# Kernel optimization log

Measured on AMD Instinct MI355X. Metric: run time of the kernel, lower is better.

## Reference

```python
import jax, jax.numpy as jnp
import numpy as np
import math

B, S, D = 2, 2048, 1024
H, DH = 16, 64          # n_heads, d_head = d_model // n_heads
WINDOW = 256            # window_size


def setup_inputs() -> dict:
    key = jax.random.key(0)
    ks = jax.random.split(key, 9)
    scale = 0.02
    return {
        "x":  jax.random.normal(ks[0], (B, S, D), dtype=jnp.float32),
        "wq": jax.random.normal(ks[1], (D, D), dtype=jnp.float32) * scale,
        "bq": jnp.zeros((D,), dtype=jnp.float32),
        "wk": jax.random.normal(ks[2], (D, D), dtype=jnp.float32) * scale,
        "bk": jnp.zeros((D,), dtype=jnp.float32),
        "wv": jax.random.normal(ks[3], (D, D), dtype=jnp.float32) * scale,
        "bv": jnp.zeros((D,), dtype=jnp.float32),
        "wo": jax.random.normal(ks[4], (D, D), dtype=jnp.float32) * scale,
        "bo": jnp.zeros((D,), dtype=jnp.float32),
    }


def reference(x, wq, bq, wk, bk, wv, bv, wo, bo):
    b, s, d = x.shape
    # QKV projections -> [b, h, s, dh]
    q = (x @ wq + bq).reshape(b, s, H, DH).transpose(0, 2, 1, 3)
    k = (x @ wk + bk).reshape(b, s, H, DH).transpose(0, 2, 1, 3)
    v = (x @ wv + bv).reshape(b, s, H, DH).transpose(0, 2, 1, 3)

    scores = jnp.einsum("bhqd,bhkd->bhqk", q, k) / math.sqrt(DH)

    # causal + local-window mask: j <= i and i - j <= window
    idx = jnp.arange(s)
    row = idx[:, None]
    col = idx[None, :]
    mask = (col <= row) & (row - col <= WINDOW)        # [s, s]
    scores = jnp.where(mask[None, None, :, :], scores, -jnp.inf)

    attn = jax.nn.softmax(scores, axis=-1)
    # torch.nan_to_num(attn, 0.0): rows always include the diagonal so no NaNs,
    # but keep faithful behavior.
    attn = jnp.nan_to_num(attn, nan=0.0)

    out = jnp.einsum("bhqk,bhkd->bhqd", attn, v)        # [b, h, s, dh]
    out = out.transpose(0, 2, 1, 3).reshape(b, s, d)
    return out @ wo + bo
```

## Files before the change

### kernel.cpp

```cpp
#include <hip/hip_runtime.h>

#define B_ 2
#define S_ 2048
#define D_ 1024
#define H_ 16
#define DH_ 64
#define WIN_ 256
#define VTS 2080

typedef __attribute__((ext_vector_type(8))) short bf16x8;
typedef __attribute__((ext_vector_type(4))) float f32x4;
typedef unsigned short u16;

#define MFMA(a, b, c) __builtin_amdgcn_mfma_f32_16x16x32_bf16((a), (b), (c), 0, 0, 0)

__device__ __forceinline__ u16 f2b(float f) {
  unsigned int u = __float_as_uint(f);
  u += 0x7fffu + ((u >> 16) & 1u);
  return (u16)(u >> 16);
}

__device__ __forceinline__ float b2f(u16 b) {
  return __uint_as_float(((unsigned int)b) << 16);
}

__device__ __forceinline__ void async_cp16(const void* g, void* l) {
  __builtin_amdgcn_global_load_lds(
      (const __attribute__((address_space(1))) void*)g,
      (__attribute__((address_space(3))) void*)l, 16, 0, 0);
}

__global__ void k_prep(const float* __restrict__ x,
                       const float* __restrict__ wq, const float* __restrict__ wk,
                       const float* __restrict__ wv, const float* __restrict__ wo,
                       u16* __restrict__ xb, u16* __restrict__ wqkvt, u16* __restrict__ wot) {
  __shared__ float tile[64][65];
  const int bx = blockIdx.x;
  const int t = threadIdx.x;
  if (bx < 1024) {
    const int t0 = (bx * 256 + t) * 4;
#pragma unroll
    for (int it = 0; it < 4; it++) {
      int i = t0 + it * 1048576;
      float4 v = *(const float4*)(x + i);
      ushort4 o;
      o.x = f2b(v.x); o.y = f2b(v.y); o.z = f2b(v.z); o.w = f2b(v.w);
      *(ushort4*)(xb + i) = o;
    }
    return;
  }
  const int tb = bx - 1024;
  const int z = tb >> 8, rest = tb & 255;
  const float* W = z == 0 ? wq : z == 1 ? wk : z == 2 ? wv : wo;
  u16* T = z < 3 ? wqkvt + (size_t)z * 1024 * 1024 : wot;
  const int bn = (rest & 15) * 64;
  const int bk = (rest >> 4) * 64;
  const int r = t >> 4;
  const int c = (t & 15) * 4;
#pragma unroll
  for (int i = 0; i < 4; i++) {
    float4 v = *(const float4*)(W + (size_t)(bk + r + i * 16) * D_ + bn + c);
    tile[c + 0][r + i * 16] = v.x;
    tile[c + 1][r + i * 16] = v.y;
    tile[c + 2][r + i * 16] = v.z;
    tile[c + 3][r + i * 16] = v.w;
  }
  __syncthreads();
  const int n = t >> 2, seg = (t & 3) * 16;
  __align__(16) u16 tmp[16];
#pragma unroll
  for (int u = 0; u < 16; u++) tmp[u] = f2b(tile[n][seg + u]);
  uint4* dst = (uint4*)(T + (size_t)(bn + n) * D_ + bk + seg);
  dst[0] = ((uint4*)tmp)[0];
  dst[1] = ((uint4*)tmp)[1];
}

__device__ __forceinline__ void gemm_core128(const u16* __restrict__ Ag, const u16* __restrict__ Btg,
                                             u16* As, u16* Bs, f32x4 (&acc)[4][4],
                                             int m0, int n0) {
  const int tid = threadIdx.x;
  const int w = tid >> 6, lane = tid & 63;
  const int quad = lane >> 4, l15 = lane & 15;
  const int wm = (w & 1) * 64, wn = (w >> 1) * 64;
  const int rowa = tid >> 3;
  const int colsw = (((tid & 7) ^ (rowa & 7)) * 8);
  const u16* ap = Ag + (size_t)(m0 + rowa) * D_ + colsw;
  const u16* bp = Btg + (size_t)(n0 + rowa) * D_ + colsw;
  u16* As0 = As + w * 512;
  u16* Bs0 = Bs + w * 512;
  const int c0 = ((quad * 8) ^ ((l15 & 7) * 8));
  for (int kb = 0; kb < D_; kb += 64) {
#pragma unroll
    for (int i = 0; i < 4; i++) {
      async_cp16(ap + kb + (size_t)(i * 32) * D_, As0 + i * 2048);
      async_cp16(bp + kb + (size_t)(i * 32) * D_, Bs0 + i * 2048);
    }
    __syncthreads();
#pragma unroll
    for (int kh = 0; kh < 2; kh++) {
      const int c = c0 ^ (kh * 32);
      bf16x8 af[4], bfr[4];
#pragma unroll
      for (int i = 0; i < 4; i++) af[i] = *(const bf16x8*)&As[(wm + i * 16 + l15) * 64 + c];
#pragma unroll
      for (int j = 0; j < 4; j++) bfr[j] = *(const bf16x8*)&Bs[(wn + j * 16 + l15) * 64 + c];
#pragma unroll
      for (int i = 0; i < 4; i++)
#pragma unroll
        for (int j = 0; j < 4; j++) acc[i][j] = MFMA(af[i], bfr[j], acc[i][j]);
    }
    __syncthreads();
  }
}

__global__ __launch_bounds__(256, 3) void k_gemm_qkv(
    const u16* __restrict__ xb, const u16* __restrict__ wqkvt,
    const float* __restrict__ bq, const float* __restrict__ bk_, const float* __restrict__ bv,
    u16* __restrict__ Qg, u16* __restrict__ Kg, u16* __restrict__ Vt) {
  __shared__ __align__(16) u16 smem[17408];
  u16* As = smem;
  u16* Bs = smem + 8192;
  const int L = blockIdx.x;
  const int xcd = L & 7, slot = L >> 3;
  const int mblk = (xcd >> 1) * 8 + (slot & 7);
  const int nblk = (xcd & 1) * 12 + (slot >> 3);
  const int n0 = nblk * 128, m0 = mblk * 128;
  const int z = n0 >> 10;
  const float* bias = z == 0 ? bq : z == 1 ? bk_ : bv;
  f32x4 acc[4][4] = {};
  gemm_core128(xb, wqkvt, As, Bs, acc, m0, n0);

  const int tid = threadIdx.x;
  const int w = tid >> 6, lane = tid & 63;
  const int quad = lane >> 4, l15 = lane & 15;
  const int wm = (w & 1) * 64, wn = (w >> 1) * 64;
  const int nloc = n0 & 1023;
  float biasv[4];
#pragma unroll
  for (int j = 0; j < 4; j++) biasv[j] = bias[nloc + wn + j * 16 + l15];
  const int b_ = m0 >> 11, sb = m0 & 2047;
  const float scale = z == 0 ? 0.125f * 1.44269504f : 1.0f;
  const int row = tid >> 4, ch = tid & 15;

  if (z < 2) {
#pragma unroll
    for (int j = 0; j < 4; j++)
#pragma unroll
      for (int i = 0; i < 4; i++)
#pragma unroll
        for (int r = 0; r < 4; r++)
          smem[(wm + i * 16 + quad * 4 + r) * 136 + wn + j * 16 + l15] =
              f2b((acc[i][j][r] + biasv[j]) * scale);
    __syncthreads();
    u16* OG = z == 0 ? Qg : Kg;
#pragma unroll
    for (int it = 0; it < 8; it++) {
      int rr = row + it * 16;
      bf16x8 v = *(const bf16x8*)&smem[rr * 136 + ch * 8];
      *(bf16x8*)(OG + (size_t)(m0 + rr) * D_ + nloc + ch * 8) = v;
    }
  } else {
#pragma unroll
    for (int j = 0; j < 4; j++)
#pragma unroll
      for (int i = 0; i < 4; i++)
#pragma unroll
        for (int r = 0; r < 4; r++)
          smem[(wn + j * 16 + l15) * 136 + wm + i * 16 + quad * 4 + r] =
              f2b(acc[i][j][r] + biasv[j]);
    __syncthreads();
#pragma unroll
    for (int it = 0; it < 8; it++) {
      int nn = nloc + row + it * 16;
      int h = nn >> 6, dh = nn & 63;
      bf16x8 v = *(const bf16x8*)&smem[(row + it * 16) * 136 + ch * 8];
      *(bf16x8*)(Vt + ((size_t)(b_ * H_ + h) * DH_ + dh) * VTS + sb + ch * 8) = v;
    }
  }
}

__global__ __launch_bounds__(256, 2) void k_gemm_out(
    const u16* __restrict__ Ab, const u16* __restrict__ wot,
    const float* __restrict__ bo, float* __restrict__ out) {
  __shared__ __align__(16) u16 smem[24576];
  u16* As = smem;
  u16* Bs = smem + 8192;
  const int L = blockIdx.x;
  const int xcd = L & 7, slot = L >> 3;
  const int mblk = xcd * 8 + (slot & 7);
  const int nblk = slot >> 3;
  const int n0 = nblk * 128, m0 = mblk * 64;
  const int tid = threadIdx.x;
  const int w = tid >> 6, lane = tid & 63;
  const int quad = lane >> 4, l15 = lane & 15;
  const int wn = w * 32;
  const int rowa = tid >> 4;
  const int gg = (tid & 15) ^ rowa;
  const u16* ap = Ab + (size_t)(m0 + rowa) * D_ + gg * 8;
  const u16* bp = wot + (size_t)(n0 + rowa) * D_ + gg * 8;
  u16* As0 = As + w * 512;
  u16* Bs0 = Bs + w * 512;
  f32x4 acc[4][2] = {};
  for (int kb = 0; kb < D_; kb += 128) {
#pragma unroll
    for (int i = 0; i < 4; i++)
      async_cp16(ap + kb + (size_t)(i * 16) * D_, As0 + i * 2048);
#pragma unroll
    for (int i = 0; i < 8; i++)
      async_cp16(bp + kb + (size_t)(i * 16) * D_, Bs0 + i * 2048);
    __syncthreads();
#pragma unroll
    for (int kh = 0; kh < 4; kh++) {
      const int cs = (((quad + 4 * kh) ^ l15) * 8);
      bf16x8 af[4], bfr[2];
#pragma unroll
      for (int i = 0; i < 4; i++) af[i] = *(const bf16x8*)&As[(i * 16 + l15) * 128 + cs];
#pragma unroll
      for (int j = 0; j < 2; j++) bfr[j] = *(const bf16x8*)&Bs[(wn + j * 16 + l15) * 128 + cs];
#pragma unroll
      for (int i = 0; i < 4; i++)
#pragma unroll
        for (int j = 0; j < 2; j++) acc[i][j] = MFMA(af[i], bfr[j], acc[i][j]);
    }
    __syncthreads();
  }
  float biasv[2];
#pragma unroll
  for (int j = 0; j < 2; j++) biasv[j] = bo[n0 + wn + j * 16 + l15];
#pragma unroll
  for (int j = 0; j < 2; j++)
#pragma unroll
    for (int i = 0; i < 4; i++)
#pragma unroll
      for (int r = 0; r < 4; r++)
        smem[(i * 16 + quad * 4 + r) * 136 + wn + j * 16 + l15] = f2b(acc[i][j][r] + biasv[j]);
  __syncthreads();
  const int row = tid >> 4, ch = tid & 15;
#pragma unroll
  for (int it = 0; it < 4; it++) {
    int rr = row + it * 16;
    bf16x8 v = *(const bf16x8*)&smem[rr * 136 + ch * 8];
    float4 f0, f1;
    f0.x = b2f((u16)v[0]); f0.y = b2f((u16)v[1]); f0.z = b2f((u16)v[2]); f0.w = b2f((u16)v[3]);
    f1.x = b2f((u16)v[4]); f1.y = b2f((u16)v[5]); f1.z = b2f((u16)v[6]); f1.w = b2f((u16)v[7]);
    float* dst = out + (size_t)(m0 + rr) * D_ + n0 + ch * 8;
    *(float4*)dst = f0;
    *(float4*)(dst + 4) = f1;
  }
}

__global__ __launch_bounds__(256, 4) void k_attn(
    const u16* __restrict__ Qg, const u16* __restrict__ Kg,
    const u16* __restrict__ Vt, u16* __restrict__ Ab) {
  __shared__ __align__(16) u16 Plds[4][16 * 72];
  const int tid = threadIdx.x;
  const int w = tid >> 6, lane = tid & 63;
  const int quad = lane >> 4, l15 = lane & 15;
  const int lid = blockIdx.x;
  const int xcd = lid & 7, slot = lid >> 3;
  const int bh = xcd * 4 + (slot & 3);
  const int qb = slot >> 2;
  const int qw = qb * 64 + w * 16;
  const int b_ = bh >> 4, h = bh & 15;

  const u16* Qbase = Qg + (size_t)(b_ * S_ + qw + l15) * D_ + h * DH_ + quad * 8;
  bf16x8 aq0 = *(const bf16x8*)Qbase;
  bf16x8 aq1 = *(const bf16x8*)(Qbase + 32);

  float lr = 0.f;
  f32x4 Oacc[4] = {};

  const u16* Kb = Kg + (size_t)b_ * S_ * D_ + h * DH_ + quad * 8;
  const u16* Vb = Vt + (size_t)bh * DH_ * VTS + (size_t)l15 * VTS + quad * 8;
  const int klo = qw >= WIN_ ? ((qw - WIN_) & ~31) : 0;
  const int q = qw + l15;
  const int srcA = l15 + ((quad & 1) ? 32 : 0);
  const int srcB = srcA + 16;

  bf16x8 k00, k01, k10, k11, v0, v1, v2, v3;
  {
    const u16* Kt0 = Kb + (size_t)(klo + l15) * D_;
    k00 = *(const bf16x8*)Kt0;
    k01 = *(const bf16x8*)(Kt0 + 32);
    k10 = *(const bf16x8*)(Kt0 + (size_t)16 * D_);
    k11 = *(const bf16x8*)(Kt0 + (size_t)16 * D_ + 32);
    const u16* Vt0 = Vb + klo;
    v0 = *(const bf16x8*)(Vt0);
    v1 = *(const bf16x8*)(Vt0 + (size_t)16 * VTS);
    v2 = *(const bf16x8*)(Vt0 + (size_t)32 * VTS);
    v3 = *(const bf16x8*)(Vt0 + (size_t)48 * VTS);
  }

  for (int k0 = klo;;) {
    const int kn = k0 + 32;
    const bool more = kn < qw + 16;
    bf16x8 nk00, nk01, nk10, nk11, nv0, nv1, nv2, nv3;
    if (more) {
      const u16* Kt0 = Kb + (size_t)(kn + l15) * D_;
      nk00 = *(const bf16x8*)Kt0;
      nk01 = *(const bf16x8*)(Kt0 + 32);
      nk10 = *(const bf16x8*)(Kt0 + (size_t)16 * D_);
      nk11 = *(const bf16x8*)(Kt0 + (size_t)16 * D_ + 32);
      const u16* Vt0 = Vb + kn;
      nv0 = *(const bf16x8*)(Vt0);
      nv1 = *(const bf16x8*)(Vt0 + (size_t)16 * VTS);
      nv2 = *(const bf16x8*)(Vt0 + (size_t)32 * VTS);
      nv3 = *(const bf16x8*)(Vt0 + (size_t)48 * VTS);
    }

    f32x4 s0 = {0.f, 0.f, 0.f, 0.f}, s1 = {0.f, 0.f, 0.f, 0.f};
    __builtin_amdgcn_s_setprio(1);
    s0 = MFMA(k00, aq0, s0);
    s0 = MFMA(k01, aq1, s0);
    s1 = MFMA(k10, aq0, s1);
    s1 = MFMA(k11, aq1, s1);
    __builtin_amdgcn_s_setprio(0);

    const bool interior = (k0 >= qw + 15 - WIN_) && (k0 + 31 <= qw);
    float e[8];
    if (interior) {
#pragma unroll
      for (int r = 0; r < 4; r++) {
        float p0 = __builtin_amdgcn_exp2f(s0[r]);
        float p1 = __builtin_amdgcn_exp2f(s1[r]);
        e[r] = p0; e[4 + r] = p1;
        lr += p0 + p1;
      }
    } else {
#pragma unroll
      for (int r = 0; r < 4; r++) {
        int key0 = k0 + quad * 4 + r;
        int key1 = key0 + 16;
        float p0 = (key0 <= q && key0 + WIN_ >= q) ? __builtin_amdgcn_exp2f(s0[r]) : 0.f;
        float p1 = (key1 <= q && key1 + WIN_ >= q) ? __builtin_amdgcn_exp2f(s1[r]) : 0.f;
        e[r] = p0; e[4 + r] = p1;
        lr += p0 + p1;
      }
    }
    unsigned int s0p01 = (unsigned)f2b(e[0]) | ((unsigned)f2b(e[1]) << 16);
    unsigned int s0p23 = (unsigned)f2b(e[2]) | ((unsigned)f2b(e[3]) << 16);
    unsigned int s1p01 = (unsigned)f2b(e[4]) | ((unsigned)f2b(e[5]) << 16);
    unsigned int s1p23 = (unsigned)f2b(e[6]) | ((unsigned)f2b(e[7]) << 16);
    unsigned int a0 = (unsigned)__shfl((int)s0p01, srcA);
    unsigned int a1 = (unsigned)__shfl((int)s0p23, srcA);
    unsigned int a2 = (unsigned)__shfl((int)s0p01, srcB);
    unsigned int a3 = (unsigned)__shfl((int)s0p23, srcB);
    unsigned int c0 = (unsigned)__shfl((int)s1p01, srcA);
    unsigned int c1 = (unsigned)__shfl((int)s1p23, srcA);
    unsigned int c2 = (unsigned)__shfl((int)s1p01, srcB);
    unsigned int c3 = (unsigned)__shfl((int)s1p23, srcB);
    union { unsigned int u[4]; bf16x8 v; } pf;
    const bool lo = quad < 2;
    pf.u[0] = lo ? a0 : c0;
    pf.u[1] = lo ? a1 : c1;
    pf.u[2] = lo ? a2 : c2;
    pf.u[3] = lo ? a3 : c3;

    __builtin_amdgcn_s_setprio(1);
    Oacc[0] = MFMA(v0, pf.v, Oacc[0]);
    Oacc[1] = MFMA(v1, pf.v, Oacc[1]);
    Oacc[2] = MFMA(v2, pf.v, Oacc[2]);
    Oacc[3] = MFMA(v3, pf.v, Oacc[3]);
    __builtin_amdgcn_s_setprio(0);

    if (!more) break;
    k00 = nk00; k01 = nk01; k10 = nk10; k11 = nk11;
    v0 = nv0; v1 = nv1; v2 = nv2; v3 = nv3;
    k0 = kn;
  }

  lr += __shfl_xor(lr, 16);
  lr += __shfl_xor(lr, 32);
  const float inv = 1.0f / lr;

  u16* P = &Plds[w][0];
#pragma unroll
  for (int j = 0; j < 4; j++)
#pragma unroll
    for (int r = 0; r < 4; r++)
      P[l15 * 72 + j * 16 + quad * 4 + r] = f2b(Oacc[j][r] * inv);
  {
    int rq = lane >> 2, cc = lane & 3;
    bf16x8 ov0 = *(const bf16x8*)&P[rq * 72 + cc * 16];
    bf16x8 ov1 = *(const bf16x8*)&P[rq * 72 + cc * 16 + 8];
    u16* dst = Ab + (size_t)(b_ * S_ + qw + rq) * D_ + h * DH_ + cc * 16;
    *(bf16x8*)dst = ov0;
    *(bf16x8*)(dst + 8) = ov1;
  }
}

extern "C" void kernel_launch(void* const* d_in, const int* in_sizes, int n_in,
                              void* d_out, int out_size, void* d_ws, size_t ws_size,
                              hipStream_t stream) {
  const float* x  = (const float*)d_in[0];
  const float* wq = (const float*)d_in[1];
  const float* bq = (const float*)d_in[2];
  const float* wk = (const float*)d_in[3];
  const float* bk = (const float*)d_in[4];
  const float* wv = (const float*)d_in[5];
  const float* bv = (const float*)d_in[6];
  const float* wo = (const float*)d_in[7];
  const float* bo = (const float*)d_in[8];

  char* ws = (char*)d_ws;
  const size_t MB = 1u << 20;
  u16* Qg    = (u16*)(ws + 0 * MB);
  u16* Kg    = (u16*)(ws + 8 * MB);
  u16* Vt    = (u16*)(ws + 16 * MB);
  u16* Ab    = (u16*)(ws + 25 * MB);
  u16* xb    = (u16*)(ws + 33 * MB);
  u16* wqkvt = (u16*)(ws + 41 * MB);
  u16* wot   = (u16*)(ws + 47 * MB);

  k_prep<<<2048, 256, 0, stream>>>(x, wq, wk, wv, wo, xb, wqkvt, wot);
  k_gemm_qkv<<<768, 256, 0, stream>>>(xb, wqkvt, bq, bk, bv, Qg, Kg, Vt);
  k_attn<<<1024, 256, 0, stream>>>(Qg, Kg, Vt, Ab);
  k_gemm_out<<<512, 256, 0, stream>>>(Ab, wot, bo, (float*)d_out);
}
```

Before: 163.2 us.

## Process two 16-row query tiles per wave to reuse K/V loads

```diff
diff --git a/kernel.cpp b/kernel.cpp
--- a/kernel.cpp
+++ b/kernel.cpp
@@ -249,10 +249,10 @@
   }
 }
 
-__global__ __launch_bounds__(256, 4) void k_attn(
+__global__ __launch_bounds__(256, 2) void k_attn(
     const u16* __restrict__ Qg, const u16* __restrict__ Kg,
     const u16* __restrict__ Vt, u16* __restrict__ Ab) {
-  __shared__ __align__(16) u16 Plds[4][16 * 72];
+  __shared__ __align__(16) u16 Plds[4][32 * 72];
   const int tid = threadIdx.x;
   const int w = tid >> 6, lane = tid & 63;
   const int quad = lane >> 4, l15 = lane & 15;
@@ -260,20 +260,24 @@
   const int xcd = lid & 7, slot = lid >> 3;
   const int bh = xcd * 4 + (slot & 3);
   const int qb = slot >> 2;
-  const int qw = qb * 64 + w * 16;
+  const int qw = qb * 128 + w * 32;
   const int b_ = bh >> 4, h = bh & 15;
 
-  const u16* Qbase = Qg + (size_t)(b_ * S_ + qw + l15) * D_ + h * DH_ + quad * 8;
-  bf16x8 aq0 = *(const bf16x8*)Qbase;
-  bf16x8 aq1 = *(const bf16x8*)(Qbase + 32);
-
-  float lr = 0.f;
-  f32x4 Oacc[4] = {};
+  const u16* QbaseA = Qg + (size_t)(b_ * S_ + qw + l15) * D_ + h * DH_ + quad * 8;
+  bf16x8 aq0 = *(const bf16x8*)QbaseA;
+  bf16x8 aq1 = *(const bf16x8*)(QbaseA + 32);
+  const u16* QbaseB = QbaseA + (size_t)16 * D_;
+  bf16x8 bq0 = *(const bf16x8*)QbaseB;
+  bf16x8 bq1 = *(const bf16x8*)(QbaseB + 32);
+
+  float lrA = 0.f, lrB = 0.f;
+  f32x4 OA[4] = {}, OB[4] = {};
 
   const u16* Kb = Kg + (size_t)b_ * S_ * D_ + h * DH_ + quad * 8;
   const u16* Vb = Vt + (size_t)bh * DH_ * VTS + (size_t)l15 * VTS + quad * 8;
-  const int klo = qw >= WIN_ ? ((qw - WIN_) & ~31) : 0;
-  const int q = qw + l15;
+  const int klo = qw >= WIN_ ? qw - WIN_ : 0;
+  const int qA = qw + l15, qB = qA + 16;
+  const int qwB = qw + 16;
   const int srcA = l15 + ((quad & 1) ? 32 : 0);
   const int srcB = srcA + 16;
 
@@ -293,7 +297,7 @@
 
   for (int k0 = klo;;) {
     const int kn = k0 + 32;
-    const bool more = kn < qw + 16;
+    const bool more = kn <= qw;
     bf16x8 nk00, nk01, nk10, nk11, nv0, nv1, nv2, nv3;
     if (more) {
       const u16* Kt0 = Kb + (size_t)(kn + l15) * D_;
@@ -308,60 +312,118 @@
       nv3 = *(const bf16x8*)(Vt0 + (size_t)48 * VTS);
     }
 
-    f32x4 s0 = {0.f, 0.f, 0.f, 0.f}, s1 = {0.f, 0.f, 0.f, 0.f};
-    __builtin_amdgcn_s_setprio(1);
-    s0 = MFMA(k00, aq0, s0);
-    s0 = MFMA(k01, aq1, s0);
-    s1 = MFMA(k10, aq0, s1);
-    s1 = MFMA(k11, aq1, s1);
-    __builtin_amdgcn_s_setprio(0);
-
-    const bool interior = (k0 >= qw + 15 - WIN_) && (k0 + 31 <= qw);
-    float e[8];
-    if (interior) {
-#pragma unroll
-      for (int r = 0; r < 4; r++) {
-        float p0 = __builtin_amdgcn_exp2f(s0[r]);
-        float p1 = __builtin_amdgcn_exp2f(s1[r]);
-        e[r] = p0; e[4 + r] = p1;
-        lr += p0 + p1;
+    const bool computeA = (k0 <= qw + 15);
+    const bool computeB = (k0 + 31 >= qwB - WIN_);
+
+    if (computeA) {
+      f32x4 s0 = {0.f, 0.f, 0.f, 0.f}, s1 = {0.f, 0.f, 0.f, 0.f};
+      __builtin_amdgcn_s_setprio(1);
+      s0 = MFMA(k00, aq0, s0);
+      s0 = MFMA(k01, aq1, s0);
+      s1 = MFMA(k10, aq0, s1);
+      s1 = MFMA(k11, aq1, s1);
+      __builtin_amdgcn_s_setprio(0);
+      const bool interior = (k0 >= qw + 15 - WIN_) && (k0 + 31 <= qw);
+      float e[8];
+      if (interior) {
+#pragma unroll
+        for (int r = 0; r < 4; r++) {
+          float p0 = __builtin_amdgcn_exp2f(s0[r]);
+          float p1 = __builtin_amdgcn_exp2f(s1[r]);
+          e[r] = p0; e[4 + r] = p1;
+          lrA += p0 + p1;
+        }
+      } else {
+#pragma unroll
+        for (int r = 0; r < 4; r++) {
+          int key0 = k0 + quad * 4 + r;
+          int key1 = key0 + 16;
+          float p0 = (key0 <= qA && key0 + WIN_ >= qA) ? __builtin_amdgcn_exp2f(s0[r]) : 0.f;
+          float p1 = (key1 <= qA && key1 + WIN_ >= qA) ? __builtin_amdgcn_exp2f(s1[r]) : 0.f;
+          e[r] = p0; e[4 + r] = p1;
+          lrA += p0 + p1;
+        }
       }
-    } else {
-#pragma unroll
-      for (int r = 0; r < 4; r++) {
-        int key0 = k0 + quad * 4 + r;
-        int key1 = key0 + 16;
-        float p0 = (key0 <= q && key0 + WIN_ >= q) ? __builtin_amdgcn_exp2f(s0[r]) : 0.f;
-        float p1 = (key1 <= q && key1 + WIN_ >= q) ? __builtin_amdgcn_exp2f(s1[r]) : 0.f;
-        e[r] = p0; e[4 + r] = p1;
-        lr += p0 + p1;
+      unsigned int s0p01 = (unsigned)f2b(e[0]) | ((unsigned)f2b(e[1]) << 16);
+      unsigned int s0p23 = (unsigned)f2b(e[2]) | ((unsigned)f2b(e[3]) << 16);
+      unsigned int s1p01 = (unsigned)f2b(e[4]) | ((unsigned)f2b(e[5]) << 16);
+      unsigned int s1p23 = (unsigned)f2b(e[6]) | ((unsigned)f2b(e[7]) << 16);
+      unsigned int a0 = (unsigned)__shfl((int)s0p01, srcA);
+      unsigned int a1 = (unsigned)__shfl((int)s0p23, srcA);
+      unsigned int a2 = (unsigned)__shfl((int)s0p01, srcB);
+      unsigned int a3 = (unsigned)__shfl((int)s0p23, srcB);
+      unsigned int c0 = (unsigned)__shfl((int)s1p01, srcA);
+      unsigned int c1 = (unsigned)__shfl((int)s1p23, srcA);
+      unsigned int c2 = (unsigned)__shfl((int)s1p01, srcB);
+      unsigned int c3 = (unsigned)__shfl((int)s1p23, srcB);
+      union { unsigned int u[4]; bf16x8 v; } pf;
+      const bool lo = quad < 2;
+      pf.u[0] = lo ? a0 : c0;
+      pf.u[1] = lo ? a1 : c1;
+      pf.u[2] = lo ? a2 : c2;
+      pf.u[3] = lo ? a3 : c3;
+      __builtin_amdgcn_s_setprio(1);
+      OA[0] = MFMA(v0, pf.v, OA[0]);
+      OA[1] = MFMA(v1, pf.v, OA[1]);
+      OA[2] = MFMA(v2, pf.v, OA[2]);
+      OA[3] = MFMA(v3, pf.v, OA[3]);
+      __builtin_amdgcn_s_setprio(0);
+    }
+
+    if (computeB) {
+      f32x4 s0 = {0.f, 0.f, 0.f, 0.f}, s1 = {0.f, 0.f, 0.f, 0.f};
+      __builtin_amdgcn_s_setprio(1);
+      s0 = MFMA(k00, bq0, s0);
+      s0 = MFMA(k01, bq1, s0);
+      s1 = MFMA(k10, bq0, s1);
+      s1 = MFMA(k11, bq1, s1);
+      __builtin_amdgcn_s_setprio(0);
+      const bool interior = (k0 >= qwB + 15 - WIN_) && (k0 + 31 <= qwB);
+      float e[8];
+      if (interior) {
+#pragma unroll
+        for (int r = 0; r < 4; r++) {
+          float p0 = __builtin_amdgcn_exp2f(s0[r]);
+          float p1 = __builtin_amdgcn_exp2f(s1[r]);
+          e[r] = p0; e[4 + r] = p1;
+          lrB += p0 + p1;
+        }
+      } else {
+#pragma unroll
+        for (int r = 0; r < 4; r++) {
+          int key0 = k0 + quad * 4 + r;
+          int key1 = key0 + 16;
+          float p0 = (key0 <= qB && key0 + WIN_ >= qB) ? __builtin_amdgcn_exp2f(s0[r]) : 0.f;
+          float p1 = (key1 <= qB && key1 + WIN_ >= qB) ? __builtin_amdgcn_exp2f(s1[r]) : 0.f;
+          e[r] = p0; e[4 + r] = p1;
+          lrB += p0 + p1;
+        }
       }
-    }
-    unsigned int s0p01 = (unsigned)f2b(e[0]) | ((unsigned)f2b(e[1]) << 16);
-    unsigned int s0p23 = (unsigned)f2b(e[2]) | ((unsigned)f2b(e[3]) << 16);
-    unsigned int s1p01 = (unsigned)f2b(e[4]) | ((unsigned)f2b(e[5]) << 16);
-    unsigned int s1p23 = (unsigned)f2b(e[6]) | ((unsigned)f2b(e[7]) << 16);
-    unsigned int a0 = (unsigned)__shfl((int)s0p01, srcA);
-    unsigned int a1 = (unsigned)__shfl((int)s0p23, srcA);
-    unsigned int a2 = (unsigned)__shfl((int)s0p01, srcB);
-    unsigned int a3 = (unsigned)__shfl((int)s0p23, srcB);
-    unsigned int c0 = (unsigned)__shfl((int)s1p01, srcA);
-    unsigned int c1 = (unsigned)__shfl((int)s1p23, srcA);
-    unsigned int c2 = (unsigned)__shfl((int)s1p01, srcB);
-    unsigned int c3 = (unsigned)__shfl((int)s1p23, srcB);
-    union { unsigned int u[4]; bf16x8 v; } pf;
-    const bool lo = quad < 2;
-    pf.u[0] = lo ? a0 : c0;
-    pf.u[1] = lo ? a1 : c1;
-    pf.u[2] = lo ? a2 : c2;
-    pf.u[3] = lo ? a3 : c3;
-
-    __builtin_amdgcn_s_setprio(1);
-    Oacc[0] = MFMA(v0, pf.v, Oacc[0]);
-    Oacc[1] = MFMA(v1, pf.v, Oacc[1]);
-    Oacc[2] = MFMA(v2, pf.v, Oacc[2]);
-    Oacc[3] = MFMA(v3, pf.v, Oacc[3]);
-    __builtin_amdgcn_s_setprio(0);
+      unsigned int s0p01 = (unsigned)f2b(e[0]) | ((unsigned)f2b(e[1]) << 16);
+      unsigned int s0p23 = (unsigned)f2b(e[2]) | ((unsigned)f2b(e[3]) << 16);
+      unsigned int s1p01 = (unsigned)f2b(e[4]) | ((unsigned)f2b(e[5]) << 16);
+      unsigned int s1p23 = (unsigned)f2b(e[6]) | ((unsigned)f2b(e[7]) << 16);
+      unsigned int a0 = (unsigned)__shfl((int)s0p01, srcA);
+      unsigned int a1 = (unsigned)__shfl((int)s0p23, srcA);
+      unsigned int a2 = (unsigned)__shfl((int)s0p01, srcB);
+      unsigned int a3 = (unsigned)__shfl((int)s0p23, srcB);
+      unsigned int c0 = (unsigned)__shfl((int)s1p01, srcA);
+      unsigned int c1 = (unsigned)__shfl((int)s1p23, srcA);
+      unsigned int c2 = (unsigned)__shfl((int)s1p01, srcB);
+      unsigned int c3 = (unsigned)__shfl((int)s1p23, srcB);
+      union { unsigned int u[4]; bf16x8 v; } pf;
+      const bool lo = quad < 2;
+      pf.u[0] = lo ? a0 : c0;
+      pf.u[1] = lo ? a1 : c1;
+      pf.u[2] = lo ? a2 : c2;
+      pf.u[3] = lo ? a3 : c3;
+      __builtin_amdgcn_s_setprio(1);
+      OB[0] = MFMA(v0, pf.v, OB[0]);
+      OB[1] = MFMA(v1, pf.v, OB[1]);
+      OB[2] = MFMA(v2, pf.v, OB[2]);
+      OB[3] = MFMA(v3, pf.v, OB[3]);
+      __builtin_amdgcn_s_setprio(0);
+    }
 
     if (!more) break;
     k00 = nk00; k01 = nk01; k10 = nk10; k11 = nk11;
@@ -369,18 +431,24 @@
     k0 = kn;
   }
 
-  lr += __shfl_xor(lr, 16);
-  lr += __shfl_xor(lr, 32);
-  const float inv = 1.0f / lr;
+  lrA += __shfl_xor(lrA, 16);
+  lrA += __shfl_xor(lrA, 32);
+  lrB += __shfl_xor(lrB, 16);
+  lrB += __shfl_xor(lrB, 32);
+  const float invA = 1.0f / lrA;
+  const float invB = 1.0f / lrB;
 
   u16* P = &Plds[w][0];
 #pragma unroll
   for (int j = 0; j < 4; j++)
 #pragma unroll
-    for (int r = 0; r < 4; r++)
-      P[l15 * 72 + j * 16 + quad * 4 + r] = f2b(Oacc[j][r] * inv);
-  {
-    int rq = lane >> 2, cc = lane & 3;
+    for (int r = 0; r < 4; r++) {
+      P[l15 * 72 + j * 16 + quad * 4 + r] = f2b(OA[j][r] * invA);
+      P[(l15 + 16) * 72 + j * 16 + quad * 4 + r] = f2b(OB[j][r] * invB);
+    }
+#pragma unroll
+  for (int it = 0; it < 2; it++) {
+    int rq = (lane >> 2) + it * 16, cc = lane & 3;
     bf16x8 ov0 = *(const bf16x8*)&P[rq * 72 + cc * 16];
     bf16x8 ov1 = *(const bf16x8*)&P[rq * 72 + cc * 16 + 8];
     u16* dst = Ab + (size_t)(b_ * S_ + qw + rq) * D_ + h * DH_ + cc * 16;
@@ -414,6 +482,6 @@
 
   k_prep<<<2048, 256, 0, stream>>>(x, wq, wk, wv, wo, xb, wqkvt, wot);
   k_gemm_qkv<<<768, 256, 0, stream>>>(xb, wqkvt, bq, bk, bv, Qg, Kg, Vt);
-  k_attn<<<1024, 256, 0, stream>>>(Qg, Kg, Vt, Ab);
+  k_attn<<<512, 256, 0, stream>>>(Qg, Kg, Vt, Ab);
   k_gemm_out<<<512, 256, 0, stream>>>(Ab, wot, bo, (float*)d_out);
 }
```

After: 153.7 us. 1.06x faster.

## Process four 16-row query strips per wave to reuse K/V tile loads

Applied to the files above, without the earlier changes.

```diff
diff --git a/kernel.cpp b/kernel.cpp
--- a/kernel.cpp
+++ b/kernel.cpp
@@ -249,31 +249,34 @@
   }
 }
 
-__global__ __launch_bounds__(256, 4) void k_attn(
+__global__ __launch_bounds__(256, 2) void k_attn(
     const u16* __restrict__ Qg, const u16* __restrict__ Kg,
     const u16* __restrict__ Vt, u16* __restrict__ Ab) {
-  __shared__ __align__(16) u16 Plds[4][16 * 72];
+  __shared__ __align__(16) u16 Plds[4][64 * 72];
   const int tid = threadIdx.x;
   const int w = tid >> 6, lane = tid & 63;
   const int quad = lane >> 4, l15 = lane & 15;
   const int lid = blockIdx.x;
   const int xcd = lid & 7, slot = lid >> 3;
   const int bh = xcd * 4 + (slot & 3);
-  const int qb = slot >> 2;
-  const int qw = qb * 64 + w * 16;
+  const int qseg = slot >> 2;
+  const int qw = qseg * 256 + w * 64;
   const int b_ = bh >> 4, h = bh & 15;
 
-  const u16* Qbase = Qg + (size_t)(b_ * S_ + qw + l15) * D_ + h * DH_ + quad * 8;
-  bf16x8 aq0 = *(const bf16x8*)Qbase;
-  bf16x8 aq1 = *(const bf16x8*)(Qbase + 32);
-
-  float lr = 0.f;
-  f32x4 Oacc[4] = {};
+  bf16x8 qf0[4], qf1[4];
+#pragma unroll
+  for (int s = 0; s < 4; s++) {
+    const u16* Qb = Qg + (size_t)(b_ * S_ + qw + s * 16 + l15) * D_ + h * DH_ + quad * 8;
+    qf0[s] = *(const bf16x8*)Qb;
+    qf1[s] = *(const bf16x8*)(Qb + 32);
+  }
+
+  float lr[4] = {0.f, 0.f, 0.f, 0.f};
+  f32x4 Oa[4][4] = {};
 
   const u16* Kb = Kg + (size_t)b_ * S_ * D_ + h * DH_ + quad * 8;
   const u16* Vb = Vt + (size_t)bh * DH_ * VTS + (size_t)l15 * VTS + quad * 8;
-  const int klo = qw >= WIN_ ? ((qw - WIN_) & ~31) : 0;
-  const int q = qw + l15;
+  const int klo = qw >= WIN_ ? qw - WIN_ : 0;
   const int srcA = l15 + ((quad & 1) ? 32 : 0);
   const int srcB = srcA + 16;
 
@@ -293,7 +296,7 @@
 
   for (int k0 = klo;;) {
     const int kn = k0 + 32;
-    const bool more = kn < qw + 16;
+    const bool more = kn <= qw + 32;
     bf16x8 nk00, nk01, nk10, nk11, nv0, nv1, nv2, nv3;
     if (more) {
       const u16* Kt0 = Kb + (size_t)(kn + l15) * D_;
@@ -308,60 +311,65 @@
       nv3 = *(const bf16x8*)(Vt0 + (size_t)48 * VTS);
     }
 
-    f32x4 s0 = {0.f, 0.f, 0.f, 0.f}, s1 = {0.f, 0.f, 0.f, 0.f};
-    __builtin_amdgcn_s_setprio(1);
-    s0 = MFMA(k00, aq0, s0);
-    s0 = MFMA(k01, aq1, s0);
-    s1 = MFMA(k10, aq0, s1);
-    s1 = MFMA(k11, aq1, s1);
-    __builtin_amdgcn_s_setprio(0);
-
-    const bool interior = (k0 >= qw + 15 - WIN_) && (k0 + 31 <= qw);
-    float e[8];
-    if (interior) {
-#pragma unroll
-      for (int r = 0; r < 4; r++) {
-        float p0 = __builtin_amdgcn_exp2f(s0[r]);
-        float p1 = __builtin_amdgcn_exp2f(s1[r]);
-        e[r] = p0; e[4 + r] = p1;
-        lr += p0 + p1;
+#pragma unroll
+    for (int s = 0; s < 4; s++) {
+      const int qws = qw + s * 16;
+      const int qs = qws + l15;
+      if (k0 <= qws + 15 && k0 + 31 >= qws - WIN_) {
+        f32x4 s0 = {0.f, 0.f, 0.f, 0.f}, s1 = {0.f, 0.f, 0.f, 0.f};
+        __builtin_amdgcn_s_setprio(1);
+        s0 = MFMA(k00, qf0[s], s0);
+        s0 = MFMA(k01, qf1[s], s0);
+        s1 = MFMA(k10, qf0[s], s1);
+        s1 = MFMA(k11, qf1[s], s1);
+        __builtin_amdgcn_s_setprio(0);
+        const bool interior = (k0 >= qws + 15 - WIN_) && (k0 + 31 <= qws);
+        float e[8];
+        if (interior) {
+#pragma unroll
+          for (int r = 0; r < 4; r++) {
+            float p0 = __builtin_amdgcn_exp2f(s0[r]);
+            float p1 = __builtin_amdgcn_exp2f(s1[r]);
+            e[r] = p0; e[4 + r] = p1;
+            lr[s] += p0 + p1;
+          }
+        } else {
+#pragma unroll
+          for (int r = 0; r < 4; r++) {
+            int key0 = k0 + quad * 4 + r;
+            int key1 = key0 + 16;
+            float p0 = (key0 <= qs && key0 + WIN_ >= qs) ? __builtin_amdgcn_exp2f(s0[r]) : 0.f;
+            float p1 = (key1 <= qs && key1 + WIN_ >= qs) ? __builtin_amdgcn_exp2f(s1[r]) : 0.f;
+            e[r] = p0; e[4 + r] = p1;
+            lr[s] += p0 + p1;
+          }
+        }
+        unsigned int s0p01 = (unsigned)f2b(e[0]) | ((unsigned)f2b(e[1]) << 16);
+        unsigned int s0p23 = (unsigned)f2b(e[2]) | ((unsigned)f2b(e[3]) << 16);
+        unsigned int s1p01 = (unsigned)f2b(e[4]) | ((unsigned)f2b(e[5]) << 16);
+        unsigned int s1p23 = (unsigned)f2b(e[6]) | ((unsigned)f2b(e[7]) << 16);
+        unsigned int a0 = (unsigned)__shfl((int)s0p01, srcA);
+        unsigned int a1 = (unsigned)__shfl((int)s0p23, srcA);
+        unsigned int a2 = (unsigned)__shfl((int)s0p01, srcB);
+        unsigned int a3 = (unsigned)__shfl((int)s0p23, srcB);
+        unsigned int c0 = (unsigned)__shfl((int)s1p01, srcA);
+        unsigned int c1 = (unsigned)__shfl((int)s1p23, srcA);
+        unsigned int c2 = (unsigned)__shfl((int)s1p01, srcB);
+        unsigned int c3 = (unsigned)__shfl((int)s1p23, srcB);
+        union { unsigned int u[4]; bf16x8 v; } pf;
+        const bool lo = quad < 2;
+        pf.u[0] = lo ? a0 : c0;
+        pf.u[1] = lo ? a1 : c1;
+        pf.u[2] = lo ? a2 : c2;
+        pf.u[3] = lo ? a3 : c3;
+        __builtin_amdgcn_s_setprio(1);
+        Oa[s][0] = MFMA(v0, pf.v, Oa[s][0]);
+        Oa[s][1] = MFMA(v1, pf.v, Oa[s][1]);
+        Oa[s][2] = MFMA(v2, pf.v, Oa[s][2]);
+        Oa[s][3] = MFMA(v3, pf.v, Oa[s][3]);
+        __builtin_amdgcn_s_setprio(0);
       }
-    } else {
-#pragma unroll
-      for (int r = 0; r < 4; r++) {
-        int key0 = k0 + quad * 4 + r;
-        int key1 = key0 + 16;
-        float p0 = (key0 <= q && key0 + WIN_ >= q) ? __builtin_amdgcn_exp2f(s0[r]) : 0.f;
-        float p1 = (key1 <= q && key1 + WIN_ >= q) ? __builtin_amdgcn_exp2f(s1[r]) : 0.f;
-        e[r] = p0; e[4 + r] = p1;
-        lr += p0 + p1;
-      }
-    }
-    unsigned int s0p01 = (unsigned)f2b(e[0]) | ((unsigned)f2b(e[1]) << 16);
-    unsigned int s0p23 = (unsigned)f2b(e[2]) | ((unsigned)f2b(e[3]) << 16);
-    unsigned int s1p01 = (unsigned)f2b(e[4]) | ((unsigned)f2b(e[5]) << 16);
-    unsigned int s1p23 = (unsigned)f2b(e[6]) | ((unsigned)f2b(e[7]) << 16);
-    unsigned int a0 = (unsigned)__shfl((int)s0p01, srcA);
-    unsigned int a1 = (unsigned)__shfl((int)s0p23, srcA);
-    unsigned int a2 = (unsigned)__shfl((int)s0p01, srcB);
-    unsigned int a3 = (unsigned)__shfl((int)s0p23, srcB);
-    unsigned int c0 = (unsigned)__shfl((int)s1p01, srcA);
-    unsigned int c1 = (unsigned)__shfl((int)s1p23, srcA);
-    unsigned int c2 = (unsigned)__shfl((int)s1p01, srcB);
-    unsigned int c3 = (unsigned)__shfl((int)s1p23, srcB);
-    union { unsigned int u[4]; bf16x8 v; } pf;
-    const bool lo = quad < 2;
-    pf.u[0] = lo ? a0 : c0;
-    pf.u[1] = lo ? a1 : c1;
-    pf.u[2] = lo ? a2 : c2;
-    pf.u[3] = lo ? a3 : c3;
-
-    __builtin_amdgcn_s_setprio(1);
-    Oacc[0] = MFMA(v0, pf.v, Oacc[0]);
-    Oacc[1] = MFMA(v1, pf.v, Oacc[1]);
-    Oacc[2] = MFMA(v2, pf.v, Oacc[2]);
-    Oacc[3] = MFMA(v3, pf.v, Oacc[3]);
-    __builtin_amdgcn_s_setprio(0);
+    }
 
     if (!more) break;
     k00 = nk00; k01 = nk01; k10 = nk10; k11 = nk11;
@@ -369,18 +377,25 @@
     k0 = kn;
   }
 
-  lr += __shfl_xor(lr, 16);
-  lr += __shfl_xor(lr, 32);
-  const float inv = 1.0f / lr;
+#pragma unroll
+  for (int s = 0; s < 4; s++) {
+    lr[s] += __shfl_xor(lr[s], 16);
+    lr[s] += __shfl_xor(lr[s], 32);
+  }
 
   u16* P = &Plds[w][0];
 #pragma unroll
-  for (int j = 0; j < 4; j++)
-#pragma unroll
-    for (int r = 0; r < 4; r++)
-      P[l15 * 72 + j * 16 + quad * 4 + r] = f2b(Oacc[j][r] * inv);
-  {
-    int rq = lane >> 2, cc = lane & 3;
+  for (int s = 0; s < 4; s++) {
+    const float inv = 1.0f / lr[s];
+#pragma unroll
+    for (int j = 0; j < 4; j++)
+#pragma unroll
+      for (int r = 0; r < 4; r++)
+        P[(l15 + s * 16) * 72 + j * 16 + quad * 4 + r] = f2b(Oa[s][j][r] * inv);
+  }
+#pragma unroll
+  for (int it = 0; it < 4; it++) {
+    int rq = (lane >> 2) + it * 16, cc = lane & 3;
     bf16x8 ov0 = *(const bf16x8*)&P[rq * 72 + cc * 16];
     bf16x8 ov1 = *(const bf16x8*)&P[rq * 72 + cc * 16 + 8];
     u16* dst = Ab + (size_t)(b_ * S_ + qw + rq) * D_ + h * DH_ + cc * 16;
@@ -414,6 +429,6 @@
 
   k_prep<<<2048, 256, 0, stream>>>(x, wq, wk, wv, wo, xb, wqkvt, wot);
   k_gemm_qkv<<<768, 256, 0, stream>>>(xb, wqkvt, bq, bk, bv, Qg, Kg, Vt);
-  k_attn<<<1024, 256, 0, stream>>>(Qg, Kg, Vt, Ab);
+  k_attn<<<256, 256, 0, stream>>>(Qg, Kg, Vt, Ab);
   k_gemm_out<<<512, 256, 0, stream>>>(Ab, wot, bo, (float*)d_out);
 }
```

Result: faster. 157.2 us (-3.7%).
